# Optimization experiments

Hardware: AMD Instinct MI355X
Metric: run time of the kernel (lower is better)

Reference implementation:

```python
import jax, jax.numpy as jnp
import numpy as np

B, C, T = 16, 256, 2048
K = 1024  # codes per layer
N_LAYERS = 3


def setup_inputs() -> dict:
    key = jax.random.key(0)
    kx, k0, k1, k2 = jax.random.split(key, 4)
    x = jax.random.normal(kx, (B, C, T), dtype=jnp.float32)
    scale = 1.0 / K
    emb0 = jax.random.uniform(k0, (K, C), minval=-scale, maxval=scale, dtype=jnp.float32)
    emb1 = jax.random.uniform(k1, (K, C), minval=-scale, maxval=scale, dtype=jnp.float32)
    emb2 = jax.random.uniform(k2, (K, C), minval=-scale, maxval=scale, dtype=jnp.float32)
    return {"x": x, "emb0": emb0, "emb1": emb1, "emb2": emb2}


def _vq_layer(x, emb):
    # x: [B, C, T], emb: [K, C]
    b, c, t = x.shape
    flat = jnp.transpose(x, (0, 2, 1)).reshape(-1, c)          # [B*T, C]
    # squared L2 distance to each code: ||f||^2 - 2 f.e + ||e||^2
    dist = (jnp.sum(flat * flat, axis=1, keepdims=True)
            - 2.0 * flat @ emb.T
            + jnp.sum(emb * emb, axis=1))                       # [B*T, K]
    idx = jnp.argmin(dist, axis=1)                              # [B*T]
    quant = jnp.transpose(emb[idx].reshape(b, t, c), (0, 2, 1)) # [B, C, T]
    sg = jax.lax.stop_gradient
    loss = jnp.mean((sg(quant) - x) ** 2) + jnp.mean((quant - sg(x)) ** 2)
    quantized = x + sg(quant - x)  # straight-through
    return quantized, loss


def reference(x, emb0, emb1, emb2):
    total_loss = jnp.float32(0.0)
    out = x
    for emb in (emb0, emb1, emb2):
        out, loss = _vq_layer(out, emb)
        total_loss = total_loss + loss
    return out, total_loss
```

## Files before the change

### kernel.cpp

```cpp
#include <hip/hip_runtime.h>
#include <stdint.h>

#define B_  16
#define C_  256
#define T_  2048
#define K_  1024
#define TOTAL_ELEMS 8388608

typedef short bf16x8 __attribute__((ext_vector_type(8)));
typedef float f32x4 __attribute__((ext_vector_type(4)));

__device__ __forceinline__ unsigned long long pack_key(float d, int idx) {
  unsigned u = __float_as_uint(d);
  u = (u & 0x80000000u) ? ~u : (u | 0x80000000u);
  return ((unsigned long long)u << 32) | (unsigned)idx;
}
__device__ __forceinline__ float unpack_dist(unsigned long long key) {
  unsigned du = (unsigned)(key >> 32);
  unsigned bits = (du & 0x80000000u) ? (du ^ 0x80000000u) : ~du;
  return __uint_as_float(bits);
}

__device__ __forceinline__ unsigned short f2bf_rne(float f) {
  unsigned u = __float_as_uint(f);
  unsigned r = u + 0x7FFFu + ((u >> 16) & 1u);
  return (unsigned short)(r >> 16);
}

__device__ __forceinline__ void gload_lds16(const void* g, void* l) {
  __builtin_amdgcn_global_load_lds(
      (const __attribute__((address_space(1))) unsigned int*)g,
      (__attribute__((address_space(3))) unsigned int*)l, 16, 0, 0);
}

__global__ __launch_bounds__(256) void prep_kernel(
    const float* __restrict__ e0, const float* __restrict__ e1,
    const float* __restrict__ e2, float* __restrict__ nrm,
    unsigned short* __restrict__ ebf, uint4* __restrict__ keysM_region,
    float* __restrict__ loss_accum, unsigned* __restrict__ counter) {
  int bid = blockIdx.x;
  int tid = threadIdx.x;
  if (bid < 12) {
    int i = bid * 256 + tid;
    const float* e = (i < 1024) ? e0 : (i < 2048) ? e1 : e2;
    const float* p = e + (size_t)(i & 1023) * C_;
    float s = 0.0f;
    for (int c = 0; c < C_; c += 4) {
      float4 v = *(const float4*)(p + c);
      s = fmaf(v.x, v.x, s); s = fmaf(v.y, v.y, s);
      s = fmaf(v.z, v.z, s); s = fmaf(v.w, v.w, s);
    }
    nrm[i] = s;
  } else if (bid < 268) {
    int i = (bid - 12) * 256 + tid;
    float4 v = *(const float4*)(e0 + (size_t)i * 4);
    unsigned lo = (unsigned)f2bf_rne(v.x) | ((unsigned)f2bf_rne(v.y) << 16);
    unsigned hi = (unsigned)f2bf_rne(v.z) | ((unsigned)f2bf_rne(v.w) << 16);
    *(uint2*)(ebf + (size_t)i * 4) = make_uint2(lo, hi);
  } else {
    int i = (bid - 268) * 256 + tid;
    keysM_region[i] = make_uint4(0xFFFFFFFFu, 0xFFFFFFFFu, 0xFFFFFFFFu, 0xFFFFFFFFu);
    if (bid == 268 && tid == 0) { *loss_accum = 0.0f; *counter = 0u; }
  }
}

__global__ __launch_bounds__(256) void map_tile_kernel(
    const float* __restrict__ e0, const float* __restrict__ e1,
    const float* __restrict__ e2, const float* __restrict__ nrm,
    unsigned long long* __restrict__ keysM) {
  __shared__ float As[16][68];
  __shared__ float Bs[16][68];
  int bid = blockIdx.x;
  int m = bid >> 8;
  int tb = bid & 255;
  int ar0 = (tb >> 4) << 6;
  int br0 = (tb & 15) << 6;
  const float* Ap = m ? e1 : e0;
  const float* Bp = m ? e2 : e1;
  const float* nB = nrm + (m + 1) * 1024;

  int tid = threadIdx.x;
  int ty = tid >> 4, tx = tid & 15;
  int srow = tid >> 2;
  int skp  = (tid & 3) << 2;

  float acc[4][4];
#pragma unroll
  for (int i = 0; i < 4; i++)
#pragma unroll
    for (int j = 0; j < 4; j++) acc[i][j] = 0.0f;

  const float* gA = Ap + (size_t)(ar0 + srow) * C_ + skp;
  const float* gB = Bp + (size_t)(br0 + srow) * C_ + skp;

  for (int kk = 0; kk < C_; kk += 16) {
    float4 av = *(const float4*)(gA + kk);
    float4 bv = *(const float4*)(gB + kk);
    __syncthreads();
    As[skp + 0][srow] = av.x; As[skp + 1][srow] = av.y;
    As[skp + 2][srow] = av.z; As[skp + 3][srow] = av.w;
    Bs[skp + 0][srow] = bv.x; Bs[skp + 1][srow] = bv.y;
    Bs[skp + 2][srow] = bv.z; Bs[skp + 3][srow] = bv.w;
    __syncthreads();
#pragma unroll
    for (int k = 0; k < 16; k++) {
      float4 a4 = *(const float4*)&As[k][ty * 4];
      float4 b4 = *(const float4*)&Bs[k][tx * 4];
      float aa[4] = {a4.x, a4.y, a4.z, a4.w};
      float bb[4] = {b4.x, b4.y, b4.z, b4.w};
#pragma unroll
      for (int i = 0; i < 4; i++)
#pragma unroll
        for (int j = 0; j < 4; j++)
          acc[i][j] = fmaf(aa[i], bb[j], acc[i][j]);
    }
  }

  float nv[4];
#pragma unroll
  for (int j = 0; j < 4; j++) nv[j] = nB[br0 + tx * 4 + j];

#pragma unroll
  for (int i = 0; i < 4; i++) {
    unsigned long long best = 0xFFFFFFFFFFFFFFFFULL;
#pragma unroll
    for (int j = 0; j < 4; j++) {
      int code = br0 + tx * 4 + j;
      float s = nv[j] - 2.0f * acc[i][j];
      unsigned long long key = pack_key(s, code);
      if (key < best) best = key;
    }
#pragma unroll
    for (int off = 1; off < 16; off <<= 1) {
      unsigned long long o = __shfl_xor(best, off, 64);
      if (o < best) best = o;
    }
    if (tx == 0)
      atomicMin(&keysM[m * 1024 + ar0 + ty * 4 + i], best);
  }
}

__global__ __launch_bounds__(512, 2) void l0_fused_kernel(
    const float* __restrict__ x, const unsigned short* __restrict__ ebf,
    const float* __restrict__ e0n, unsigned long long* __restrict__ keys,
    float* __restrict__ loss_accum) {
  extern __shared__ char smem[];
  char* Abuf = smem;
  char* Bbuf = smem + 65536;

  int tid = threadIdx.x;
  int l = tid & 63, w = tid >> 6;
  int row0 = blockIdx.x << 7;

  {
    int row = tid & 127;
    int cg  = tid >> 7;
    int bb  = blockIdx.x >> 4;
    int t0  = (blockIdx.x & 15) << 7;
    const float* xb = x + (size_t)bb * (C_ * T_) + t0 + row;
    float sumsq = 0.0f;
#pragma unroll
    for (int i = 0; i < 8; i++) {
      int c0 = cg * 64 + i * 8;
      float v[8];
#pragma unroll
      for (int u = 0; u < 8; u++) {
        v[u] = xb[(size_t)(c0 + u) * T_];
        sumsq = fmaf(v[u], v[u], sumsq);
      }
      unsigned pk[4];
#pragma unroll
      for (int j = 0; j < 4; j++)
        pk[j] = (unsigned)f2bf_rne(v[2 * j]) | ((unsigned)f2bf_rne(v[2 * j + 1]) << 16);
      int cc = c0 >> 3;
      char* dst = Abuf + row * 512 + ((((cc >> 2)) ^ ((row >> 2) & 1)) << 6) +
                  (((cc & 3) ^ (row & 3)) << 4);
      *(uint4*)dst = make_uint4(pk[0], pk[1], pk[2], pk[3]);
    }
    for (int off = 32; off > 0; off >>= 1) sumsq += __shfl_down(sumsq, off, 64);
    float* red = (float*)(Bbuf + 16384);
    if (l == 0) red[w] = sumsq;
    __syncthreads();
    if (tid == 0) {
      float s = 0.0f;
#pragma unroll
      for (int i = 0; i < 8; i++) s += red[i];
      atomicAdd(loss_accum, s);
    }
  }

#define STAGEB(d_, p_, kk_) do {                                             \
    char* bbase = Bbuf + (d_) * 16384 + (w * 32) * 64;                       \
    _Pragma("unroll")                                                        \
    for (int j_ = 0; j_ < 2; j_++) {                                         \
      int code_ = (p_) * 256 + w * 32 + j_ * 16 + (l >> 2);                  \
      int seg_ = (l & 3) ^ ((l >> 2) & 3) ^ ((l >> 4) & 3);                  \
      gload_lds16(ebf + (((size_t)code_) << 8) + ((kk_) << 5) + (seg_ << 3), \
                  bbase + j_ * 1024);                                        \
    } } while (0)

  STAGEB(0, 0, 0);
  __syncthreads();

  int wr = w >> 2, wc = w & 3;
  int lr = l & 15, lg = l >> 4;
  int akb1 = (lr >> 2) & 1;
  int asegoff = (lg ^ (lr & 3)) << 4;
  int bsegoff = (lg ^ ((lr ^ (lr >> 2)) & 3)) << 4;

  f32x4 acc[4][4];
  float bestv[4][4];
  int   bestm[4][4];
#pragma unroll
  for (int mi = 0; mi < 4; mi++)
#pragma unroll
    for (int r = 0; r < 4; r++) { bestv[mi][r] = -1e30f; bestm[mi][r] = 0; }

  int d = 0;
  for (int p = 0; p < 4; p++) {
#pragma unroll
    for (int ni = 0; ni < 4; ni++) {
      float iv = -0.5f * e0n[p * 256 + wc * 64 + ni * 16 + lr];
      f32x4 ivv = {iv, iv, iv, iv};
#pragma unroll
      for (int mi = 0; mi < 4; mi++) acc[mi][ni] = ivv;
    }
#pragma unroll
    for (int kk = 0; kk < 8; kk++) {
      if (kk < 7) { STAGEB(d ^ 1, p, kk + 1); }
      else if (p < 3) { STAGEB(d ^ 1, p + 1, 0); }
      bf16x8 aF[4], bF[4];
#pragma unroll
      for (int mi = 0; mi < 4; mi++)
        aF[mi] = *(const bf16x8*)(Abuf + (wr * 64 + mi * 16 + lr) * 512 +
                                  ((kk ^ akb1) << 6) + asegoff);
#pragma unroll
      for (int ni = 0; ni < 4; ni++)
        bF[ni] = *(const bf16x8*)(Bbuf + d * 16384 +
                                  (wc * 64 + ni * 16 + lr) * 64 + bsegoff);
#pragma unroll
      for (int mi = 0; mi < 4; mi++)
#pragma unroll
        for (int ni = 0; ni < 4; ni++)
          acc[mi][ni] = __builtin_amdgcn_mfma_f32_16x16x32_bf16(
              aF[mi], bF[ni], acc[mi][ni], 0, 0, 0);
      __syncthreads();
      d ^= 1;
    }
#pragma unroll
    for (int mi = 0; mi < 4; mi++)
#pragma unroll
      for (int r = 0; r < 4; r++)
#pragma unroll
        for (int ni = 0; ni < 4; ni++) {
          float v = acc[mi][ni][r];
          if (v > bestv[mi][r]) { bestv[mi][r] = v; bestm[mi][r] = p * 4 + ni; }
        }
  }
#undef STAGEB

  unsigned long long (*kred)[4] = (unsigned long long(*)[4])Bbuf;
#pragma unroll
  for (int mi = 0; mi < 4; mi++)
#pragma unroll
    for (int r = 0; r < 4; r++) {
      float sdist = -2.0f * bestv[mi][r];
      int m = bestm[mi][r];
      int code = ((m >> 2) << 8) | (wc << 6) | ((m & 3) << 4) | lr;
      unsigned long long key = pack_key(sdist, code);
#pragma unroll
      for (int off = 1; off < 16; off <<= 1) {
        unsigned long long o = __shfl_xor(key, off, 64);
        if (o < key) key = o;
      }
      if (lr == 0) kred[wr * 64 + mi * 16 + lg * 4 + r][wc] = key;
    }
  __syncthreads();
  if (tid < 128) {
    unsigned long long b0 = kred[tid][0], b1 = kred[tid][1];
    unsigned long long b2 = kred[tid][2], b3 = kred[tid][3];
    if (b1 < b0) b0 = b1;
    if (b3 < b2) b2 = b3;
    keys[row0 + tid] = b0 < b2 ? b0 : b2;
  }
}

__global__ __launch_bounds__(256) void finish_kernel(
    const float* __restrict__ emb2,
    const unsigned long long* __restrict__ keys,
    const unsigned long long* __restrict__ keysM,
    const float* __restrict__ nrm,
    float* __restrict__ out, float* __restrict__ loss_accum,
    unsigned* __restrict__ counter) {
  __shared__ int code2_l[64];
  __shared__ float rloss[64];
  int tid = threadIdx.x;
  int b  = blockIdx.x >> 5;
  int t0 = (blockIdx.x & 31) << 6;
  int tt = tid & 63, w = tid >> 6;

  if (w == 0) {
    unsigned long long key0 = keys[(size_t)b * T_ + t0 + tt];
    int idx0 = (int)(key0 & 0xFFFFFFFFULL);
    float s0 = unpack_dist(key0);
    unsigned long long k1 = keysM[idx0];
    int c1 = (int)(k1 & 0xFFFFFFFFULL);
    unsigned long long k2 = keysM[1024 + c1];
    code2_l[tt] = (int)(k2 & 0xFFFFFFFFULL);
    rloss[tt] = s0 + nrm[idx0] + unpack_dist(k1) + nrm[1024 + c1] + unpack_dist(k2);
  }
  __syncthreads();

  float* ob = out + ((size_t)b << 19);
  int code2 = code2_l[tt];
  const float* e2row = emb2 + (size_t)code2 * C_;
  for (int c4 = w * 64; c4 < w * 64 + 64; c4 += 4) {
    float4 ev = *(const float4*)(e2row + c4);
    float evv[4] = {ev.x, ev.y, ev.z, ev.w};
#pragma unroll
    for (int u = 0; u < 4; u++)
      ob[(size_t)(c4 + u) * T_ + t0 + tt] = evv[u];
  }
  if (w == 0) {
    float tot = rloss[tt];
    for (int off = 32; off > 0; off >>= 1)
      tot += __shfl_down(tot, off, 64);
    if (tt == 0) atomicAdd(loss_accum, tot);
  }
  if (tid == 0) {
    __threadfence();
    unsigned old = atomicAdd(counter, 1u);
    if (old == 511u) {
      float L = atomicAdd(loss_accum, 0.0f);
      out[TOTAL_ELEMS] = 2.0f * L / 8388608.0f;
    }
  }
}

extern "C" void kernel_launch(void* const* d_in, const int* in_sizes, int n_in,
                              void* d_out, int out_size, void* d_ws, size_t ws_size,
                              hipStream_t stream) {
  const float* x  = (const float*)d_in[0];
  const float* e0 = (const float*)d_in[1];
  const float* e1 = (const float*)d_in[2];
  const float* e2 = (const float*)d_in[3];
  float* out = (float*)d_out;
  char* ws = (char*)d_ws;

  unsigned long long* keys  = (unsigned long long*)ws;
  unsigned long long* keysM = (unsigned long long*)(ws + 262144);
  float* nrm  = (float*)(ws + 278528);
  float* loss_accum = (float*)(ws + 290816);
  unsigned* counter = (unsigned*)(ws + 290820);
  unsigned short* embbf = (unsigned short*)(ws + 294912);

  prep_kernel<<<272, 256, 0, stream>>>(e0, e1, e2, nrm, embbf, (uint4*)keysM,
                                       loss_accum, counter);
  l0_fused_kernel<<<256, 512, 98304, stream>>>(x, embbf, nrm, keys, loss_accum);
  map_tile_kernel<<<512, 256, 0, stream>>>(e0, e1, e2, nrm, keysM);
  finish_kernel<<<512, 256, 0, stream>>>(e2, keys, keysM, nrm, out, loss_accum, counter);
}
```

Before: 92.49 us.

## Load codebook B fragments directly from global into registers, drop LDS staging

The bf16 codebook is stored in a fragment-friendly transposed layout (channel-group major), so each lane can load its MFMA B operand straight from global/L2 into a register double-buffer. This removes the B-tile staging through LDS and the per-k-step __syncthreads barriers. The A tile moves to an unswizzled channel-group-major LDS layout and dynamic LDS shrinks from 96 KB to 64 KB. The trade-off is that every wave re-reads the codebook from cache rather than sharing it through LDS, and the new A layout may add LDS bank conflicts.

```diff
diff --git a/kernel.cpp b/kernel.cpp
--- a/kernel.cpp
+++ b/kernel.cpp
@@ -27,16 +27,10 @@
   return (unsigned short)(r >> 16);
 }
 
-__device__ __forceinline__ void gload_lds16(const void* g, void* l) {
-  __builtin_amdgcn_global_load_lds(
-      (const __attribute__((address_space(1))) unsigned int*)g,
-      (__attribute__((address_space(3))) unsigned int*)l, 16, 0, 0);
-}
-
 __global__ __launch_bounds__(256) void prep_kernel(
     const float* __restrict__ e0, const float* __restrict__ e1,
     const float* __restrict__ e2, float* __restrict__ nrm,
-    unsigned short* __restrict__ ebf, uint4* __restrict__ keysM_region,
+    unsigned short* __restrict__ ebt, uint4* __restrict__ keysM_region,
     float* __restrict__ loss_accum, unsigned* __restrict__ counter) {
   int bid = blockIdx.x;
   int tid = threadIdx.x;
@@ -52,11 +46,13 @@
     }
     nrm[i] = s;
   } else if (bid < 268) {
-    int i = (bid - 12) * 256 + tid;
-    float4 v = *(const float4*)(e0 + (size_t)i * 4);
+    int code = (bid - 12) * 4 + (tid >> 6);
+    int c = (tid & 63) * 4;
+    float4 v = *(const float4*)(e0 + (size_t)code * C_ + c);
     unsigned lo = (unsigned)f2bf_rne(v.x) | ((unsigned)f2bf_rne(v.y) << 16);
     unsigned hi = (unsigned)f2bf_rne(v.z) | ((unsigned)f2bf_rne(v.w) << 16);
-    *(uint2*)(ebf + (size_t)i * 4) = make_uint2(lo, hi);
+    int cc = c >> 3, half = (c >> 2) & 1;
+    *(uint2*)(ebt + ((size_t)cc * 1024 + code) * 8 + half * 4) = make_uint2(lo, hi);
   } else {
     int i = (bid - 268) * 256 + tid;
     keysM_region[i] = make_uint4(0xFFFFFFFFu, 0xFFFFFFFFu, 0xFFFFFFFFu, 0xFFFFFFFFu);
@@ -141,15 +137,17 @@
 }
 
 __global__ __launch_bounds__(512, 2) void l0_fused_kernel(
-    const float* __restrict__ x, const unsigned short* __restrict__ ebf,
+    const float* __restrict__ x, const unsigned short* __restrict__ ebt,
     const float* __restrict__ e0n, unsigned long long* __restrict__ keys,
     float* __restrict__ loss_accum) {
-  extern __shared__ char smem[];
-  char* Abuf = smem;
-  char* Bbuf = smem + 65536;
+  extern __shared__ char Abuf[];
+  __shared__ unsigned long long kred[128][4];
+  __shared__ float red[8];
 
   int tid = threadIdx.x;
   int l = tid & 63, w = tid >> 6;
+  int lr = l & 15, lg = l >> 4;
+  int wr = w >> 2, wc = w & 3;
   int row0 = blockIdx.x << 7;
 
   {
@@ -173,40 +171,35 @@
       for (int j = 0; j < 4; j++)
         pk[j] = (unsigned)f2bf_rne(v[2 * j]) | ((unsigned)f2bf_rne(v[2 * j + 1]) << 16);
       int cc = c0 >> 3;
-      char* dst = Abuf + row * 512 + ((((cc >> 2)) ^ ((row >> 2) & 1)) << 6) +
-                  (((cc & 3) ^ (row & 3)) << 4);
-      *(uint4*)dst = make_uint4(pk[0], pk[1], pk[2], pk[3]);
+      *(uint4*)(Abuf + ((size_t)cc * 128 + row) * 16) =
+          make_uint4(pk[0], pk[1], pk[2], pk[3]);
     }
     for (int off = 32; off > 0; off >>= 1) sumsq += __shfl_down(sumsq, off, 64);
-    float* red = (float*)(Bbuf + 16384);
     if (l == 0) red[w] = sumsq;
-    __syncthreads();
-    if (tid == 0) {
-      float s = 0.0f;
-#pragma unroll
-      for (int i = 0; i < 8; i++) s += red[i];
-      atomicAdd(loss_accum, s);
-    }
-  }
-
-#define STAGEB(d_, p_, kk_) do {                                             \
-    char* bbase = Bbuf + (d_) * 16384 + (w * 32) * 64;                       \
+  }
+  __syncthreads();
+  if (tid == 0) {
+    float s = 0.0f;
+#pragma unroll
+    for (int i = 0; i < 8; i++) s += red[i];
+    atomicAdd(loss_accum, s);
+  }
+
+  float nv[4][4];
+#pragma unroll
+  for (int p = 0; p < 4; p++)
+#pragma unroll
+    for (int ni = 0; ni < 4; ni++)
+      nv[p][ni] = e0n[p * 256 + wc * 64 + ni * 16 + lr];
+
+  const unsigned short* pB = ebt + ((size_t)lg * 1024 + wc * 64 + lr) * 8;
+
+#define LOADB(d_, p_, kk_) do {                                              \
     _Pragma("unroll")                                                        \
-    for (int j_ = 0; j_ < 2; j_++) {                                         \
-      int code_ = (p_) * 256 + w * 32 + j_ * 16 + (l >> 2);                  \
-      int seg_ = (l & 3) ^ ((l >> 2) & 3) ^ ((l >> 4) & 3);                  \
-      gload_lds16(ebf + (((size_t)code_) << 8) + ((kk_) << 5) + (seg_ << 3), \
-                  bbase + j_ * 1024);                                        \
-    } } while (0)
-
-  STAGEB(0, 0, 0);
-  __syncthreads();
-
-  int wr = w >> 2, wc = w & 3;
-  int lr = l & 15, lg = l >> 4;
-  int akb1 = (lr >> 2) & 1;
-  int asegoff = (lg ^ (lr & 3)) << 4;
-  int bsegoff = (lg ^ ((lr ^ (lr >> 2)) & 3)) << 4;
+    for (int ni_ = 0; ni_ < 4; ni_++)                                        \
+      bbuf[d_][ni_] = *(const bf16x8*)(pB +                                  \
+          ((size_t)(kk_) * 4096 + (p_) * 256 + ni_ * 16) * 8);               \
+  } while (0)
 
   f32x4 acc[4][4];
   float bestv[4][4];
@@ -216,36 +209,34 @@
 #pragma unroll
     for (int r = 0; r < 4; r++) { bestv[mi][r] = -1e30f; bestm[mi][r] = 0; }
 
-  int d = 0;
+  bf16x8 bbuf[2][4];
+  LOADB(0, 0, 0);
+
+#pragma unroll
   for (int p = 0; p < 4; p++) {
 #pragma unroll
     for (int ni = 0; ni < 4; ni++) {
-      float iv = -0.5f * e0n[p * 256 + wc * 64 + ni * 16 + lr];
+      float iv = -0.5f * nv[p][ni];
       f32x4 ivv = {iv, iv, iv, iv};
 #pragma unroll
       for (int mi = 0; mi < 4; mi++) acc[mi][ni] = ivv;
     }
 #pragma unroll
     for (int kk = 0; kk < 8; kk++) {
-      if (kk < 7) { STAGEB(d ^ 1, p, kk + 1); }
-      else if (p < 3) { STAGEB(d ^ 1, p + 1, 0); }
-      bf16x8 aF[4], bF[4];
+      int cur = kk & 1, nxt = cur ^ 1;
+      if (kk < 7)      { LOADB(nxt, p, kk + 1); }
+      else if (p < 3)  { LOADB(nxt, p + 1, 0); }
+      bf16x8 aF[4];
 #pragma unroll
       for (int mi = 0; mi < 4; mi++)
-        aF[mi] = *(const bf16x8*)(Abuf + (wr * 64 + mi * 16 + lr) * 512 +
-                                  ((kk ^ akb1) << 6) + asegoff);
-#pragma unroll
-      for (int ni = 0; ni < 4; ni++)
-        bF[ni] = *(const bf16x8*)(Bbuf + d * 16384 +
-                                  (wc * 64 + ni * 16 + lr) * 64 + bsegoff);
+        aF[mi] = *(const bf16x8*)(Abuf + (size_t)(kk * 4 + lg) * 2048 +
+                                  (wr * 64 + mi * 16 + lr) * 16);
 #pragma unroll
       for (int mi = 0; mi < 4; mi++)
 #pragma unroll
         for (int ni = 0; ni < 4; ni++)
           acc[mi][ni] = __builtin_amdgcn_mfma_f32_16x16x32_bf16(
-              aF[mi], bF[ni], acc[mi][ni], 0, 0, 0);
-      __syncthreads();
-      d ^= 1;
+              aF[mi], bbuf[cur][ni], acc[mi][ni], 0, 0, 0);
     }
 #pragma unroll
     for (int mi = 0; mi < 4; mi++)
@@ -257,9 +248,8 @@
           if (v > bestv[mi][r]) { bestv[mi][r] = v; bestm[mi][r] = p * 4 + ni; }
         }
   }
-#undef STAGEB
-
-  unsigned long long (*kred)[4] = (unsigned long long(*)[4])Bbuf;
+#undef LOADB
+
 #pragma unroll
   for (int mi = 0; mi < 4; mi++)
 #pragma unroll
@@ -352,11 +342,11 @@
   float* nrm  = (float*)(ws + 278528);
   float* loss_accum = (float*)(ws + 290816);
   unsigned* counter = (unsigned*)(ws + 290820);
-  unsigned short* embbf = (unsigned short*)(ws + 294912);
-
-  prep_kernel<<<272, 256, 0, stream>>>(e0, e1, e2, nrm, embbf, (uint4*)keysM,
+  unsigned short* ebt = (unsigned short*)(ws + 294912);
+
+  prep_kernel<<<272, 256, 0, stream>>>(e0, e1, e2, nrm, ebt, (uint4*)keysM,
                                        loss_accum, counter);
-  l0_fused_kernel<<<256, 512, 98304, stream>>>(x, embbf, nrm, keys, loss_accum);
+  l0_fused_kernel<<<256, 512, 65536, stream>>>(x, ebt, nrm, keys, loss_accum);
   map_tile_kernel<<<512, 256, 0, stream>>>(e0, e1, e2, nrm, keysM);
   finish_kernel<<<512, 256, 0, stream>>>(e2, keys, keysM, nrm, out, loss_accum, counter);
 }
```

After: 157.2 us. 69.9% more time.
